# Kernel optimization log

Hardware: AMD Instinct MI355X
Metric: run time of the kernel (lower is better)

Reference implementation:

```python
import jax, jax.numpy as jnp
import numpy as np

NEG_SLOPE = 0.2

def gat_conv(x, src, dst, W, a_src, a_dst, b, n_nodes):
    # x: [N, Fin] -> h: [N, Fout]; edges (src->dst) incl. self-loops
    h = x @ W                                   # [N, Fout]
    as_ = h @ a_src                             # [N] per-node source score
    ad_ = h @ a_dst                             # [N] per-node dest score
    e = jax.nn.leaky_relu(as_[src] + ad_[dst], NEG_SLOPE)   # [E]
    # segment softmax over edges sharing the same destination
    e_max = jax.ops.segment_max(e, dst, num_segments=n_nodes)
    e_exp = jnp.exp(e - e_max[dst])
    e_sum = jax.ops.segment_sum(e_exp, dst, num_segments=n_nodes)
    alpha = e_exp / (e_sum[dst] + 1e-16)        # [E]
    out = jax.ops.segment_sum(alpha[:, None] * h[src], dst, num_segments=n_nodes)
    return out + b

def setup_inputs() -> dict:
    key = jax.random.key(0)
    ks = jax.random.split(key, 12)
    N, E, Fin, H = 100000, 3200000, 128, 32
    def g(k, shape, scale):
        return jax.random.normal(k, shape, dtype=jnp.float32) * scale
    return {
        "x": g(ks[0], (N, Fin), 1.0),
        "edge_index": jax.random.randint(ks[1], (2, E), 0, N, dtype=jnp.int32),
        "W1": g(ks[2], (Fin, H), 1.0 / np.sqrt(Fin)),
        "att_src1": g(ks[3], (H,), 1.0 / np.sqrt(H)),
        "att_dst1": g(ks[4], (H,), 1.0 / np.sqrt(H)),
        "b1": jnp.zeros((H,), jnp.float32),
        "W2": g(ks[5], (H, H), 1.0 / np.sqrt(H)),
        "att_src2": g(ks[6], (H,), 1.0 / np.sqrt(H)),
        "att_dst2": g(ks[7], (H,), 1.0 / np.sqrt(H)),
        "b2": jnp.zeros((H,), jnp.float32),
        "Wf": g(ks[8], (H, H), 1.0 / np.sqrt(H)),
        "bf": jnp.zeros((H,), jnp.float32),
    }

def reference(x, edge_index, W1, att_src1, att_dst1, b1, W2, att_src2, att_dst2, b2, Wf, bf):
    n_nodes = x.shape[0]
    loops = jnp.arange(n_nodes, dtype=edge_index.dtype)
    src = jnp.concatenate([edge_index[0], loops])  # add_self_loops=True (PyG default)
    dst = jnp.concatenate([edge_index[1], loops])
    h = jax.nn.relu(gat_conv(x, src, dst, W1, att_src1, att_dst1, b1, n_nodes))
    h = jax.nn.relu(gat_conv(h, src, dst, W2, att_src2, att_dst2, b2, n_nodes))
    return h @ Wf + bf
```

## Files before the change

kernel.cpp:

```cpp
#include <hip/hip_runtime.h>

#define NEG_SLOPE 0.2f
#define BK_SH 8
#define BK_SZ 256
#define MAXBUCK 512
#define EPB 8192

typedef _Float16 half8 __attribute__((ext_vector_type(8)));
typedef float f32x4 __attribute__((ext_vector_type(4)));

__global__ __launch_bounds__(256) void k_castW(const float* __restrict__ W,
                                               _Float16* __restrict__ Wt,
                                               int K) {
  for (int i = threadIdx.x; i < K * 32; i += 256) {
    int k = i >> 5, f = i & 31;
    Wt[f * K + k] = (_Float16)W[i];
  }
}

__global__ __launch_bounds__(256) void k_feat1(
    const float* __restrict__ x, const _Float16* __restrict__ Wt,
    const float* __restrict__ a_src, const float* __restrict__ a_dst,
    _Float16* __restrict__ Hh, float* __restrict__ as_, float* __restrict__ ad_,
    int N) {
  int w = threadIdx.x >> 6;
  int lane = threadIdx.x & 63;
  int base = (blockIdx.x * 4 + w) * 16;
  if (base >= N) return;
  int row16 = lane & 15;
  int kg = lane >> 4;
  f32x4 acc0 = {0.f, 0.f, 0.f, 0.f};
  f32x4 acc1 = {0.f, 0.f, 0.f, 0.f};
  const float* xr = x + (size_t)(base + row16) * 128 + kg * 8;
#pragma unroll
  for (int kt = 0; kt < 4; ++kt) {
    float4 u0 = *reinterpret_cast<const float4*>(xr + kt * 32);
    float4 u1 = *reinterpret_cast<const float4*>(xr + kt * 32 + 4);
    half8 a;
    a[0] = (_Float16)u0.x; a[1] = (_Float16)u0.y;
    a[2] = (_Float16)u0.z; a[3] = (_Float16)u0.w;
    a[4] = (_Float16)u1.x; a[5] = (_Float16)u1.y;
    a[6] = (_Float16)u1.z; a[7] = (_Float16)u1.w;
    half8 b0 = *reinterpret_cast<const half8*>(Wt + (size_t)row16 * 128 +
                                               kt * 32 + kg * 8);
    half8 b1 = *reinterpret_cast<const half8*>(Wt + (size_t)(16 + row16) * 128 +
                                               kt * 32 + kg * 8);
    acc0 = __builtin_amdgcn_mfma_f32_16x16x32_f16(a, b0, acc0, 0, 0, 0);
    acc1 = __builtin_amdgcn_mfma_f32_16x16x32_f16(a, b1, acc1, 0, 0, 0);
  }
  float aS0 = a_src[row16], aS1 = a_src[16 + row16];
  float aD0 = a_dst[row16], aD1 = a_dst[16 + row16];
  float tS[4], tD[4];
#pragma unroll
  for (int r = 0; r < 4; ++r) {
    int row = base + kg * 4 + r;
    Hh[(size_t)row * 32 + row16] = (_Float16)acc0[r];
    Hh[(size_t)row * 32 + 16 + row16] = (_Float16)acc1[r];
    tS[r] = acc0[r] * aS0 + acc1[r] * aS1;
    tD[r] = acc0[r] * aD0 + acc1[r] * aD1;
  }
#pragma unroll
  for (int off = 1; off <= 8; off <<= 1) {
#pragma unroll
    for (int r = 0; r < 4; ++r) {
      tS[r] += __shfl_xor(tS[r], off, 64);
      tD[r] += __shfl_xor(tD[r], off, 64);
    }
  }
  if (row16 == 0) {
#pragma unroll
    for (int r = 0; r < 4; ++r) {
      as_[base + kg * 4 + r] = tS[r];
      ad_[base + kg * 4 + r] = tD[r];
    }
  }
}

__global__ __launch_bounds__(256) void k_zero(int* __restrict__ p, int n) {
  int i = blockIdx.x * 256 + threadIdx.x;
  if (i < n) p[i] = 0;
}

__global__ __launch_bounds__(256) void k_bhist(const int* __restrict__ ei,
                                               int E, int* __restrict__ bcnt,
                                               int* __restrict__ hmatT,
                                               int nb, int nbuck) {
  __shared__ int h[MAXBUCK];
  for (int i = threadIdx.x; i < nbuck; i += 256) h[i] = 0;
  __syncthreads();
  long base = (long)blockIdx.x * EPB;
#pragma unroll 4
  for (int i = 0; i < EPB / 256; ++i) {
    long e = base + i * 256 + threadIdx.x;
    if (e < E) atomicAdd(&h[ei[E + e] >> BK_SH], 1);
  }
  __syncthreads();
  for (int i = threadIdx.x; i < nbuck; i += 256) {
    hmatT[(size_t)i * nb + blockIdx.x] = h[i];
    if (h[i]) atomicAdd(&bcnt[i], h[i]);
  }
}

__global__ __launch_bounds__(1024) void k_scan(const int* __restrict__ bcnt,
                                               int* __restrict__ boff,
                                               int* __restrict__ ptr, int nbuck,
                                               int N, int E) {
  __shared__ int s[1024];
  int t = threadIdx.x;
  int v = (t < nbuck) ? bcnt[t] : 0;
  s[t] = v;
  __syncthreads();
  for (int off = 1; off < 1024; off <<= 1) {
    int x = (t >= off) ? s[t - off] : 0;
    __syncthreads();
    s[t] += x;
    __syncthreads();
  }
  if (t < nbuck) boff[t] = s[t] - v;
  if (t == 0) {
    boff[nbuck] = E;
    ptr[N] = E;
  }
}

__global__ __launch_bounds__(256) void k_colscan(const int* __restrict__ hmatT,
                                                 int* __restrict__ lbgT,
                                                 const int* __restrict__ boff,
                                                 int nb, int nbuck) {
  int wid = (blockIdx.x * 256 + threadIdx.x) >> 6;
  int lane = threadIdx.x & 63;
  if (wid >= nbuck) return;
  const int* row = hmatT + (size_t)wid * nb;
  int* orow = lbgT + (size_t)wid * nb;
  int base = boff[wid];
  for (int c = 0; c < nb; c += 64) {
    int v = (c + lane < nb) ? row[c + lane] : 0;
    int s = v;
#pragma unroll
    for (int off = 1; off < 64; off <<= 1) {
      int x = __shfl_up(s, off, 64);
      if (lane >= off) s += x;
    }
    if (c + lane < nb) orow[c + lane] = base + s - v;
    base += __shfl(s, 63, 64);
  }
}

__global__ __launch_bounds__(256) void k_binA(
    const int* __restrict__ ei, int E, const int* __restrict__ hmatT,
    const int* __restrict__ lbgT, unsigned* __restrict__ packed, int nb,
    int nbuck) {
  __shared__ int h[MAXBUCK];
  __shared__ int lbase[MAXBUCK];
  __shared__ int lb[MAXBUCK];
  __shared__ int cur[MAXBUCK];
  __shared__ int psum[256];
  __shared__ unsigned rec[EPB];
  __shared__ unsigned char bkt[EPB];
  int t = threadIdx.x;
  for (int i = t; i < MAXBUCK; i += 256) {
    h[i] = (i < nbuck) ? hmatT[(size_t)i * nb + blockIdx.x] : 0;
    lbase[i] = (i < nbuck) ? lbgT[(size_t)i * nb + blockIdx.x] : 0;
  }
  __syncthreads();
  long base = (long)blockIdx.x * EPB;
  int cnt = (int)((E - base) < EPB ? (E - base) : EPB);
  int a0 = h[2 * t], a1 = h[2 * t + 1];
  psum[t] = a0 + a1;
  __syncthreads();
  for (int off = 1; off < 256; off <<= 1) {
    int x = (t >= off) ? psum[t - off] : 0;
    __syncthreads();
    psum[t] += x;
    __syncthreads();
  }
  int pex = psum[t] - (a0 + a1);
  lb[2 * t] = pex;
  lb[2 * t + 1] = pex + a0;
  cur[2 * t] = pex;
  cur[2 * t + 1] = pex + a0;
  __syncthreads();
#pragma unroll 4
  for (int i = 0; i < EPB / 256; ++i) {
    int e = i * 256 + t;
    if (e < cnt) {
      int s = ei[base + e], d = ei[E + base + e];
      int b = d >> BK_SH;
      int pos = atomicAdd(&cur[b], 1);
      rec[pos] = ((unsigned)s << 8) | (unsigned)(d & (BK_SZ - 1));
      bkt[pos] = (unsigned char)b;
    }
  }
  __syncthreads();
  for (int i = t; i < cnt; i += 256) {
    int b0 = bkt[i];
    int b = (i >= lb[b0] && i < cur[b0]) ? b0 : b0 + 256;
    packed[(size_t)lbase[b] + (i - lb[b])] = rec[i];
  }
}

__global__ __launch_bounds__(256) void k_binB(const unsigned* __restrict__ packed,
                                              const int* __restrict__ boff,
                                              int* __restrict__ ptr,
                                              int* __restrict__ srcs, int N) {
  int b = blockIdx.x;
  int beg = boff[b], end = boff[b + 1];
  int t = threadIdx.x;
  __shared__ int lcnt[BK_SZ];
  __shared__ int sc[BK_SZ];
  __shared__ int lcur[BK_SZ];
  lcnt[t] = 0;
  __syncthreads();
  for (int i = beg + t; i < end; i += 256)
    atomicAdd(&lcnt[packed[i] & (BK_SZ - 1)], 1);
  __syncthreads();
  int v = lcnt[t];
  sc[t] = v;
  __syncthreads();
  for (int off = 1; off < 256; off <<= 1) {
    int x = (t >= off) ? sc[t - off] : 0;
    __syncthreads();
    sc[t] += x;
    __syncthreads();
  }
  int excl = sc[t] - v;
  int node = (b << BK_SH) + t;
  if (node < N) ptr[node] = beg + excl;
  lcur[t] = excl;
  __syncthreads();
  for (int i = beg + t; i < end; i += 256) {
    unsigned p = packed[i];
    int slot = atomicAdd(&lcur[p & (BK_SZ - 1)], 1);
    srcs[(size_t)beg + slot] = (int)(p >> 8);
  }
}

__global__ __launch_bounds__(256) void k_fill(const int* __restrict__ srcs,
                                              const float* __restrict__ as_,
                                              int2* __restrict__ rec, int E) {
  int i = blockIdx.x * 256 + threadIdx.x;
  int stride = gridDim.x * 256;
  for (int e = i; e < E; e += stride) {
    int s = srcs[e];
    int2 r;
    r.x = s;
    r.y = __float_as_int(as_[s]);
    rec[e] = r;
  }
}

template <int MODE>
__global__ __launch_bounds__(256) void k_gatherT(
    const int* __restrict__ ptr, const int2* __restrict__ rec,
    const _Float16* __restrict__ Hh, const float* __restrict__ as_,
    const float* __restrict__ ad_, const float* __restrict__ b,
    const float* __restrict__ Wx, const float* __restrict__ aS2p,
    const float* __restrict__ aD2p, const float* __restrict__ bfp,
    _Float16* __restrict__ Hh2, float* __restrict__ as2v,
    float* __restrict__ ad2v, float* __restrict__ OUT, int N) {
  __shared__ float sW[32 * 32];
  __shared__ float sO[8][33];
  for (int i = threadIdx.x; i < 32 * 32; i += 256) sW[i] = Wx[i];
  int g = threadIdx.x >> 5;
  int lane = threadIdx.x & 31;
  int sub = lane >> 2;
  int q = lane & 3;
  int d = blockIdx.x * 8 + g;
  int dc = d < N ? d : N - 1;
  float ad_d = ad_[dc];
  float acc[8] = {0.f, 0.f, 0.f, 0.f, 0.f, 0.f, 0.f, 0.f};
  float sumw = 0.f;
  int beg = ptr[dc], end = ptr[dc + 1];
  bool v0 = sub < end - beg;
  int2 r0 = v0 ? rec[beg + sub] : make_int2(dc, 0);
  half8 hv0 = *reinterpret_cast<const half8*>(Hh + (size_t)r0.x * 32 + q * 8);
  bool v1 = sub < end - (beg + 8);
  int2 r1 = v1 ? rec[beg + 8 + sub] : make_int2(dc, 0);
  half8 hv1 = *reinterpret_cast<const half8*>(Hh + (size_t)r1.x * 32 + q * 8);
  int nb8 = (end - beg + 7) >> 3;
  int j = beg;
#pragma unroll 2
  for (int it = 0; it < nb8; ++it) {
    int jn = j + 16;
    bool v2 = sub < end - jn;
    int2 r2 = v2 ? rec[jn + sub] : make_int2(dc, 0);
    half8 hv2 = *reinterpret_cast<const half8*>(Hh + (size_t)r2.x * 32 + q * 8);
    float sc2 = __int_as_float(r0.y) + ad_d;
    float el = sc2 > 0.f ? sc2 : NEG_SLOPE * sc2;
    float w = v0 ? __expf(el) : 0.f;
#pragma unroll
    for (int i = 0; i < 8; ++i) acc[i] += w * (float)hv0[i];
    sumw += w;
    j = jn - 8;
    v0 = v1; r0 = r1; hv0 = hv1;
    v1 = v2; r1 = r2; hv1 = hv2;
  }
#pragma unroll
  for (int off = 4; off <= 16; off <<= 1) {
#pragma unroll
    for (int i = 0; i < 8; ++i) acc[i] += __shfl_xor(acc[i], off, 32);
    sumw += __shfl_xor(sumw, off, 32);
  }
  if (sub == 0) {
    float s0 = as_[dc] + ad_d;
    float e0 = s0 > 0.f ? s0 : NEG_SLOPE * s0;
    float w0 = __expf(e0);
    half8 hs = *reinterpret_cast<const half8*>(Hh + (size_t)dc * 32 + q * 8);
#pragma unroll
    for (int i = 0; i < 8; ++i) acc[i] += w0 * (float)hs[i];
    sumw += w0;
    float inv = 1.f / (sumw + 1e-16f);
#pragma unroll
    for (int i = 0; i < 8; ++i)
      sO[g][q * 8 + i] = fmaxf(acc[i] * inv + b[q * 8 + i], 0.f);
  }
  __syncthreads();
  float accf = (MODE == 1) ? bfp[lane] : 0.f;
#pragma unroll
  for (int k = 0; k < 32; ++k) accf += sO[g][k] * sW[k * 32 + lane];
  if (MODE == 1) {
    if (d < N) OUT[(size_t)d * 32 + lane] = accf;
  } else {
    if (d < N) Hh2[(size_t)d * 32 + lane] = (_Float16)accf;
    float vs = accf * aS2p[lane];
    float vd = accf * aD2p[lane];
#pragma unroll
    for (int off = 1; off < 32; off <<= 1) {
      vs += __shfl_xor(vs, off, 32);
      vd += __shfl_xor(vd, off, 32);
    }
    if (lane == 0 && d < N) {
      as2v[d] = vs;
      ad2v[d] = vd;
    }
  }
}

extern "C" void kernel_launch(void* const* d_in, const int* in_sizes, int n_in,
                              void* d_out, int out_size, void* d_ws,
                              size_t ws_size, hipStream_t stream) {
  const float* x = (const float*)d_in[0];
  const int* ei = (const int*)d_in[1];
  const float* W1 = (const float*)d_in[2];
  const float* as1 = (const float*)d_in[3];
  const float* ad1 = (const float*)d_in[4];
  const float* b1 = (const float*)d_in[5];
  const float* W2 = (const float*)d_in[6];
  const float* as2 = (const float*)d_in[7];
  const float* ad2 = (const float*)d_in[8];
  const float* b2 = (const float*)d_in[9];
  const float* Wf = (const float*)d_in[10];
  const float* bf = (const float*)d_in[11];
  float* out = (float*)d_out;

  const int H = in_sizes[3];
  const int FIN = in_sizes[2] / H;
  const int N = in_sizes[0] / FIN;
  const int E = in_sizes[1] / 2;
  const int nbuck = (N + BK_SZ - 1) >> BK_SH;
  (void)n_in; (void)out_size; (void)ws_size; (void)H;

  const int nodeBlocks = (N + 7) / 8;
  const int binBlocks = (E + EPB - 1) / EPB;
  const int mfmaBlocks = (N / 16 + 3) / 4;

  size_t r0 = (size_t)E * 8;
  char* basep = (char*)d_ws;
  unsigned* packed = (unsigned*)basep;
  int2* recb = (int2*)basep;
  char* p = basep + r0;
  _Float16* Hh1 = (_Float16*)p;  p += (size_t)N * 32 * 2;
  _Float16* Hh2 = (_Float16*)p;  p += (size_t)N * 32 * 2;
  _Float16* Wt1 = (_Float16*)p;  p += (size_t)128 * 32 * 2;
  float* asv = (float*)p;        p += (size_t)N * 4;
  float* adv = (float*)p;        p += (size_t)N * 4;
  float* asv2 = (float*)p;       p += (size_t)N * 4;
  float* adv2 = (float*)p;       p += (size_t)N * 4;
  int* ptr = (int*)p;            p += (size_t)(N + 1) * 4;
  int* srcs = (int*)p;           p += (size_t)E * 4;
  int* bcnt = (int*)p;           p += (size_t)nbuck * 4;
  int* boff = (int*)p;           p += (size_t)(nbuck + 1) * 4;
  int* hmatT = (int*)p;          p += (size_t)binBlocks * nbuck * 4;
  int* lbgT = (int*)p;

  k_zero<<<(nbuck + 255) / 256, 256, 0, stream>>>(bcnt, nbuck);
  k_bhist<<<binBlocks, 256, 0, stream>>>(ei, E, bcnt, hmatT, binBlocks, nbuck);
  k_scan<<<1, 1024, 0, stream>>>(bcnt, boff, ptr, nbuck, N, E);
  k_colscan<<<(nbuck * 64 + 255) / 256, 256, 0, stream>>>(hmatT, lbgT, boff,
                                                          binBlocks, nbuck);
  k_binA<<<binBlocks, 256, 0, stream>>>(ei, E, hmatT, lbgT, packed, binBlocks,
                                        nbuck);
  k_binB<<<nbuck, 256, 0, stream>>>(packed, boff, ptr, srcs, N);

  k_castW<<<1, 256, 0, stream>>>(W1, Wt1, 128);

  k_feat1<<<mfmaBlocks, 256, 0, stream>>>(x, Wt1, as1, ad1, Hh1, asv, adv, N);
  k_fill<<<2048, 256, 0, stream>>>(srcs, asv, recb, E);
  k_gatherT<0><<<nodeBlocks, 256, 0, stream>>>(ptr, recb, Hh1, asv, adv, b1,
                                               W2, as2, ad2, nullptr, Hh2,
                                               asv2, adv2, nullptr, N);

  k_fill<<<2048, 256, 0, stream>>>(srcs, asv2, recb, E);
  k_gatherT<1><<<nodeBlocks, 256, 0, stream>>>(ptr, recb, Hh2, asv2, adv2, b2,
                                               Wf, nullptr, nullptr, bf,
                                               nullptr, nullptr, nullptr, out,
                                               N);
}
```

Measured before the change: 248.2 us.

## Drop k_fill record pass; gather source scores inline with fp16 dot2 accumulation

Removes the k_fill kernels that packed (src, as_[src]) records. The gather kernel now reads srcs directly and fetches as_[src] itself. Each lane handles two edges per iteration and accumulates them with packed fp16 fdot2, which halves the loop trip count and deepens prefetch to four edges in flight. This saves two full passes over E edges and an 8-byte record write and read per edge. The cost is an extra dependent random gather of as_ inside the hot loop and lower weight precision, since weights are rounded to fp16 with round-toward-zero.

```diff
diff --git a/kernel.cpp b/kernel.cpp
--- a/kernel.cpp
+++ b/kernel.cpp
@@ -7,6 +7,7 @@
 #define EPB 8192
 
 typedef _Float16 half8 __attribute__((ext_vector_type(8)));
+typedef _Float16 h2 __attribute__((ext_vector_type(2)));
 typedef float f32x4 __attribute__((ext_vector_type(4)));
 
 __global__ __launch_bounds__(256) void k_castW(const float* __restrict__ W,
@@ -235,23 +236,9 @@
   }
 }
 
-__global__ __launch_bounds__(256) void k_fill(const int* __restrict__ srcs,
-                                              const float* __restrict__ as_,
-                                              int2* __restrict__ rec, int E) {
-  int i = blockIdx.x * 256 + threadIdx.x;
-  int stride = gridDim.x * 256;
-  for (int e = i; e < E; e += stride) {
-    int s = srcs[e];
-    int2 r;
-    r.x = s;
-    r.y = __float_as_int(as_[s]);
-    rec[e] = r;
-  }
-}
-
 template <int MODE>
 __global__ __launch_bounds__(256) void k_gatherT(
-    const int* __restrict__ ptr, const int2* __restrict__ rec,
+    const int* __restrict__ ptr, const int* __restrict__ srcs,
     const _Float16* __restrict__ Hh, const float* __restrict__ as_,
     const float* __restrict__ ad_, const float* __restrict__ b,
     const float* __restrict__ Wx, const float* __restrict__ aS2p,
@@ -271,29 +258,56 @@
   float acc[8] = {0.f, 0.f, 0.f, 0.f, 0.f, 0.f, 0.f, 0.f};
   float sumw = 0.f;
   int beg = ptr[dc], end = ptr[dc + 1];
-  bool v0 = sub < end - beg;
-  int2 r0 = v0 ? rec[beg + sub] : make_int2(dc, 0);
-  half8 hv0 = *reinterpret_cast<const half8*>(Hh + (size_t)r0.x * 32 + q * 8);
-  bool v1 = sub < end - (beg + 8);
-  int2 r1 = v1 ? rec[beg + 8 + sub] : make_int2(dc, 0);
-  half8 hv1 = *reinterpret_cast<const half8*>(Hh + (size_t)r1.x * 32 + q * 8);
-  int nb8 = (end - beg + 7) >> 3;
-  int j = beg;
-#pragma unroll 2
-  for (int it = 0; it < nb8; ++it) {
-    int jn = j + 16;
-    bool v2 = sub < end - jn;
-    int2 r2 = v2 ? rec[jn + sub] : make_int2(dc, 0);
-    half8 hv2 = *reinterpret_cast<const half8*>(Hh + (size_t)r2.x * 32 + q * 8);
-    float sc2 = __int_as_float(r0.y) + ad_d;
-    float el = sc2 > 0.f ? sc2 : NEG_SLOPE * sc2;
-    float w = v0 ? __expf(el) : 0.f;
-#pragma unroll
-    for (int i = 0; i < 8; ++i) acc[i] += w * (float)hv0[i];
-    sumw += w;
-    j = jn - 8;
-    v0 = v1; r0 = r1; hv0 = hv1;
-    v1 = v2; r1 = r2; hv1 = hv2;
+  const _Float16* Hq = Hh + q * 8;
+
+  bool vA0, vB0, vA1, vB1;
+  int sA0, sB0, sA1, sB1;
+  float aA0, aB0, aA1, aB1;
+  half8 hA0, hB0, hA1, hB1;
+
+  vA0 = beg + sub < end;          vB0 = beg + 8 + sub < end;
+  sA0 = vA0 ? srcs[beg + sub] : dc;
+  sB0 = vB0 ? srcs[beg + 8 + sub] : dc;
+  aA0 = as_[sA0]; aB0 = as_[sB0];
+  hA0 = *reinterpret_cast<const half8*>(Hq + (size_t)sA0 * 32);
+  hB0 = *reinterpret_cast<const half8*>(Hq + (size_t)sB0 * 32);
+  vA1 = beg + 16 + sub < end;     vB1 = beg + 24 + sub < end;
+  sA1 = vA1 ? srcs[beg + 16 + sub] : dc;
+  sB1 = vB1 ? srcs[beg + 24 + sub] : dc;
+  aA1 = as_[sA1]; aB1 = as_[sB1];
+  hA1 = *reinterpret_cast<const half8*>(Hq + (size_t)sA1 * 32);
+  hB1 = *reinterpret_cast<const half8*>(Hq + (size_t)sB1 * 32);
+
+  int nit = (end - beg + 15) >> 4;
+  int jb = beg;
+  for (int it = 0; it < nit; ++it) {
+    int jn = jb + 32;
+    bool vA2 = jn + sub < end, vB2 = jn + 8 + sub < end;
+    int sA2 = vA2 ? srcs[jn + sub] : dc;
+    int sB2 = vB2 ? srcs[jn + 8 + sub] : dc;
+    float aA2 = as_[sA2], aB2 = as_[sB2];
+    half8 hA2 = *reinterpret_cast<const half8*>(Hq + (size_t)sA2 * 32);
+    half8 hB2 = *reinterpret_cast<const half8*>(Hq + (size_t)sB2 * 32);
+    float scA = aA0 + ad_d, scB = aB0 + ad_d;
+    float elA = scA > 0.f ? scA : NEG_SLOPE * scA;
+    float elB = scB > 0.f ? scB : NEG_SLOPE * scB;
+    float wA = vA0 ? __expf(elA) : 0.f;
+    float wB = vB0 ? __expf(elB) : 0.f;
+    auto pk = __builtin_amdgcn_cvt_pkrtz(wA, wB);
+    h2 wpk = __builtin_bit_cast(h2, pk);
+#pragma unroll
+    for (int i = 0; i < 8; ++i) {
+      h2 hp;
+      hp[0] = hA0[i];
+      hp[1] = hB0[i];
+      acc[i] = __builtin_amdgcn_fdot2(wpk, hp, acc[i], false);
+    }
+    sumw += wA + wB;
+    jb += 16;
+    vA0 = vA1; vB0 = vB1; sA0 = sA1; sB0 = sB1;
+    aA0 = aA1; aB0 = aB1; hA0 = hA1; hB0 = hB1;
+    vA1 = vA2; vB1 = vB2; sA1 = sA2; sB1 = sB2;
+    aA1 = aA2; aB1 = aB2; hA1 = hA2; hB1 = hB2;
   }
 #pragma unroll
   for (int off = 4; off <= 16; off <<= 1) {
@@ -305,7 +319,7 @@
     float s0 = as_[dc] + ad_d;
     float e0 = s0 > 0.f ? s0 : NEG_SLOPE * s0;
     float w0 = __expf(e0);
-    half8 hs = *reinterpret_cast<const half8*>(Hh + (size_t)dc * 32 + q * 8);
+    half8 hs = *reinterpret_cast<const half8*>(Hq + (size_t)dc * 32);
 #pragma unroll
     for (int i = 0; i < 8; ++i) acc[i] += w0 * (float)hs[i];
     sumw += w0;
@@ -364,11 +378,9 @@
   const int binBlocks = (E + EPB - 1) / EPB;
   const int mfmaBlocks = (N / 16 + 3) / 4;
 
-  size_t r0 = (size_t)E * 8;
   char* basep = (char*)d_ws;
   unsigned* packed = (unsigned*)basep;
-  int2* recb = (int2*)basep;
-  char* p = basep + r0;
+  char* p = basep + (size_t)E * 4;
   _Float16* Hh1 = (_Float16*)p;  p += (size_t)N * 32 * 2;
   _Float16* Hh2 = (_Float16*)p;  p += (size_t)N * 32 * 2;
   _Float16* Wt1 = (_Float16*)p;  p += (size_t)128 * 32 * 2;
@@ -395,13 +407,11 @@
   k_castW<<<1, 256, 0, stream>>>(W1, Wt1, 128);
 
   k_feat1<<<mfmaBlocks, 256, 0, stream>>>(x, Wt1, as1, ad1, Hh1, asv, adv, N);
-  k_fill<<<2048, 256, 0, stream>>>(srcs, asv, recb, E);
-  k_gatherT<0><<<nodeBlocks, 256, 0, stream>>>(ptr, recb, Hh1, asv, adv, b1,
+  k_gatherT<0><<<nodeBlocks, 256, 0, stream>>>(ptr, srcs, Hh1, asv, adv, b1,
                                                W2, as2, ad2, nullptr, Hh2,
                                                asv2, adv2, nullptr, N);
 
-  k_fill<<<2048, 256, 0, stream>>>(srcs, asv2, recb, E);
-  k_gatherT<1><<<nodeBlocks, 256, 0, stream>>>(ptr, recb, Hh2, asv2, adv2, b2,
+  k_gatherT<1><<<nodeBlocks, 256, 0, stream>>>(ptr, srcs, Hh2, asv2, adv2, b2,
                                                Wf, nullptr, nullptr, bf,
                                                nullptr, nullptr, nullptr, out,
                                                N);
```

Result: faster. 215.7 us (-13.1%).

## Drop k_fill record pass; gather source scores directly with deeper prefetch

Applied to the files above, without the earlier changes.

Removes the k_fill kernel, which built an int2 (src, score) record array per edge before each gather layer. The gather kernels now read the int src index and then load as_[src] themselves, which adds a dependent random load but cuts two full passes over E edges and halves edge-array traffic. The software prefetch depth goes from two to three edge groups (unroll 3) to hide the extra load latency. Scores are pre-scaled by log2(e) so exp2f can replace __expf, which is mathematically equivalent since leaky_relu commutes with positive scaling.

```diff
diff --git a/kernel.cpp b/kernel.cpp
--- a/kernel.cpp
+++ b/kernel.cpp
@@ -1,6 +1,7 @@
 #include <hip/hip_runtime.h>
 
 #define NEG_SLOPE 0.2f
+#define LOG2E 1.44269504f
 #define BK_SH 8
 #define BK_SZ 256
 #define MAXBUCK 512
@@ -70,8 +71,8 @@
   if (row16 == 0) {
 #pragma unroll
     for (int r = 0; r < 4; ++r) {
-      as_[base + kg * 4 + r] = tS[r];
-      ad_[base + kg * 4 + r] = tD[r];
+      as_[base + kg * 4 + r] = tS[r] * LOG2E;
+      ad_[base + kg * 4 + r] = tD[r] * LOG2E;
     }
   }
 }
@@ -235,23 +236,9 @@
   }
 }
 
-__global__ __launch_bounds__(256) void k_fill(const int* __restrict__ srcs,
-                                              const float* __restrict__ as_,
-                                              int2* __restrict__ rec, int E) {
-  int i = blockIdx.x * 256 + threadIdx.x;
-  int stride = gridDim.x * 256;
-  for (int e = i; e < E; e += stride) {
-    int s = srcs[e];
-    int2 r;
-    r.x = s;
-    r.y = __float_as_int(as_[s]);
-    rec[e] = r;
-  }
-}
-
 template <int MODE>
 __global__ __launch_bounds__(256) void k_gatherT(
-    const int* __restrict__ ptr, const int2* __restrict__ rec,
+    const int* __restrict__ ptr, const int* __restrict__ srcs,
     const _Float16* __restrict__ Hh, const float* __restrict__ as_,
     const float* __restrict__ ad_, const float* __restrict__ b,
     const float* __restrict__ Wx, const float* __restrict__ aS2p,
@@ -271,29 +258,38 @@
   float acc[8] = {0.f, 0.f, 0.f, 0.f, 0.f, 0.f, 0.f, 0.f};
   float sumw = 0.f;
   int beg = ptr[dc], end = ptr[dc + 1];
+  const _Float16* Hq = Hh + q * 8;
   bool v0 = sub < end - beg;
-  int2 r0 = v0 ? rec[beg + sub] : make_int2(dc, 0);
-  half8 hv0 = *reinterpret_cast<const half8*>(Hh + (size_t)r0.x * 32 + q * 8);
+  int s0_ = v0 ? srcs[beg + sub] : dc;
+  float a0_ = as_[s0_];
+  half8 h0_ = *reinterpret_cast<const half8*>(Hq + (size_t)s0_ * 32);
   bool v1 = sub < end - (beg + 8);
-  int2 r1 = v1 ? rec[beg + 8 + sub] : make_int2(dc, 0);
-  half8 hv1 = *reinterpret_cast<const half8*>(Hh + (size_t)r1.x * 32 + q * 8);
+  int s1_ = v1 ? srcs[beg + 8 + sub] : dc;
+  float a1_ = as_[s1_];
+  half8 h1_ = *reinterpret_cast<const half8*>(Hq + (size_t)s1_ * 32);
+  bool v2 = sub < end - (beg + 16);
+  int s2_ = v2 ? srcs[beg + 16 + sub] : dc;
+  float a2_ = as_[s2_];
+  half8 h2_ = *reinterpret_cast<const half8*>(Hq + (size_t)s2_ * 32);
   int nb8 = (end - beg + 7) >> 3;
   int j = beg;
-#pragma unroll 2
+#pragma unroll 3
   for (int it = 0; it < nb8; ++it) {
-    int jn = j + 16;
-    bool v2 = sub < end - jn;
-    int2 r2 = v2 ? rec[jn + sub] : make_int2(dc, 0);
-    half8 hv2 = *reinterpret_cast<const half8*>(Hh + (size_t)r2.x * 32 + q * 8);
-    float sc2 = __int_as_float(r0.y) + ad_d;
+    int jn = j + 24;
+    bool v3 = sub < end - jn;
+    int s3_ = v3 ? srcs[jn + sub] : dc;
+    float a3_ = as_[s3_];
+    half8 h3_ = *reinterpret_cast<const half8*>(Hq + (size_t)s3_ * 32);
+    float sc2 = a0_ + ad_d;
     float el = sc2 > 0.f ? sc2 : NEG_SLOPE * sc2;
-    float w = v0 ? __expf(el) : 0.f;
-#pragma unroll
-    for (int i = 0; i < 8; ++i) acc[i] += w * (float)hv0[i];
+    float w = v0 ? exp2f(el) : 0.f;
+#pragma unroll
+    for (int i = 0; i < 8; ++i) acc[i] += w * (float)h0_[i];
     sumw += w;
-    j = jn - 8;
-    v0 = v1; r0 = r1; hv0 = hv1;
-    v1 = v2; r1 = r2; hv1 = hv2;
+    j += 8;
+    v0 = v1; s0_ = s1_; a0_ = a1_; h0_ = h1_;
+    v1 = v2; s1_ = s2_; a1_ = a2_; h1_ = h2_;
+    v2 = v3; s2_ = s3_; a2_ = a3_; h2_ = h3_;
   }
 #pragma unroll
   for (int off = 4; off <= 16; off <<= 1) {
@@ -304,8 +300,8 @@
   if (sub == 0) {
     float s0 = as_[dc] + ad_d;
     float e0 = s0 > 0.f ? s0 : NEG_SLOPE * s0;
-    float w0 = __expf(e0);
-    half8 hs = *reinterpret_cast<const half8*>(Hh + (size_t)dc * 32 + q * 8);
+    float w0 = exp2f(e0);
+    half8 hs = *reinterpret_cast<const half8*>(Hq + (size_t)dc * 32);
 #pragma unroll
     for (int i = 0; i < 8; ++i) acc[i] += w0 * (float)hs[i];
     sumw += w0;
@@ -330,8 +326,8 @@
       vd += __shfl_xor(vd, off, 32);
     }
     if (lane == 0 && d < N) {
-      as2v[d] = vs;
-      ad2v[d] = vd;
+      as2v[d] = vs * LOG2E;
+      ad2v[d] = vd * LOG2E;
     }
   }
 }
@@ -364,11 +360,9 @@
   const int binBlocks = (E + EPB - 1) / EPB;
   const int mfmaBlocks = (N / 16 + 3) / 4;
 
-  size_t r0 = (size_t)E * 8;
   char* basep = (char*)d_ws;
   unsigned* packed = (unsigned*)basep;
-  int2* recb = (int2*)basep;
-  char* p = basep + r0;
+  char* p = basep + (size_t)E * 4;
   _Float16* Hh1 = (_Float16*)p;  p += (size_t)N * 32 * 2;
   _Float16* Hh2 = (_Float16*)p;  p += (size_t)N * 32 * 2;
   _Float16* Wt1 = (_Float16*)p;  p += (size_t)128 * 32 * 2;
@@ -395,13 +389,11 @@
   k_castW<<<1, 256, 0, stream>>>(W1, Wt1, 128);
 
   k_feat1<<<mfmaBlocks, 256, 0, stream>>>(x, Wt1, as1, ad1, Hh1, asv, adv, N);
-  k_fill<<<2048, 256, 0, stream>>>(srcs, asv, recb, E);
-  k_gatherT<0><<<nodeBlocks, 256, 0, stream>>>(ptr, recb, Hh1, asv, adv, b1,
+  k_gatherT<0><<<nodeBlocks, 256, 0, stream>>>(ptr, srcs, Hh1, asv, adv, b1,
                                                W2, as2, ad2, nullptr, Hh2,
                                                asv2, adv2, nullptr, N);
 
-  k_fill<<<2048, 256, 0, stream>>>(srcs, asv2, recb, E);
-  k_gatherT<1><<<nodeBlocks, 256, 0, stream>>>(ptr, recb, Hh2, asv2, adv2, b2,
+  k_gatherT<1><<<nodeBlocks, 256, 0, stream>>>(ptr, srcs, Hh2, asv2, adv2, b2,
                                                Wf, nullptr, nullptr, bf,
                                                nullptr, nullptr, nullptr, out,
                                                N);
```

Result: faster. 230.0 us (-7.3%).
